# Optimization experiments

Hardware: AMD Instinct MI355X
Metric: run time of the kernel (lower is better)

## Reference

```python
import jax, jax.numpy as jnp
import numpy as np

D_MODEL = 1024
D_INNER = 2048
D_STATE = 16
D_CONV = 4
DT_RANK = 64  # ceil(d_model/16)


def _silu(v):
    return v * jax.nn.sigmoid(v)


def setup_inputs() -> dict:
    key = jax.random.key(0)
    ks = jax.random.split(key, 10)
    b, L = 2, 2048
    x = jax.random.normal(ks[0], (b, L, D_MODEL), jnp.float32)
    dt_vals = jax.random.uniform(ks[1], (b, L, 1), jnp.float32)
    W_in = jax.random.normal(ks[2], (D_MODEL, 2 * D_INNER), jnp.float32) * D_MODEL ** -0.5
    conv_w = jax.random.normal(ks[3], (D_INNER, D_CONV), jnp.float32) * D_CONV ** -0.5
    conv_b = jnp.zeros((D_INNER,), jnp.float32)
    W_x = jax.random.normal(ks[4], (D_INNER, DT_RANK + 2 * D_STATE), jnp.float32) * D_INNER ** -0.5
    std = DT_RANK ** -0.5
    W_dt = jax.random.uniform(ks[5], (1, D_INNER), jnp.float32, -std, std)
    dt = jnp.exp(jax.random.uniform(ks[6], (D_INNER,), jnp.float32)
                 * (np.log(0.1) - np.log(0.001)) + np.log(0.001))
    dt = jnp.clip(dt, 1e-4)
    b_dt = dt + jnp.log(-jnp.expm1(-dt))  # inverse-softplus init
    A_log = jnp.log(jnp.broadcast_to(jnp.arange(1, D_STATE + 1, dtype=jnp.float32),
                                     (D_INNER, D_STATE)))
    D_param = jnp.ones((D_INNER,), jnp.float32)
    W_out = jax.random.normal(ks[7], (D_INNER, D_MODEL), jnp.float32) * D_INNER ** -0.5
    return {"x": x, "dt_vals": dt_vals, "W_in": W_in, "conv_w": conv_w,
            "conv_b": conv_b, "W_x": W_x, "W_dt": W_dt, "b_dt": b_dt,
            "A_log": A_log, "D_param": D_param, "W_out": W_out}


def reference(x, dt_vals, W_in, conv_w, conv_b, W_x, W_dt, b_dt, A_log, D_param, W_out):
    b, L, _ = x.shape
    xz = x @ W_in                              # (b, L, 2*d_inner)
    xi, z = jnp.split(xz, 2, axis=-1)          # each (b, L, d_inner)
    # Causal depthwise conv1d (torch pads d_conv-1 both sides then slices [:seq])
    xp = jnp.pad(xi, ((0, 0), (D_CONV - 1, 0), (0, 0))).transpose(0, 2, 1)  # (b, di, L+k-1)
    xc = jax.lax.conv_general_dilated(
        xp, conv_w[:, None, :], window_strides=(1,), padding='VALID',
        dimension_numbers=('NCH', 'OIH', 'NCH'), feature_group_count=D_INNER)  # (b, di, L)
    xc = _silu(xc.transpose(0, 2, 1) + conv_b)  # (b, L, d_inner)

    x_dbl = xc @ W_x                            # (b, L, dt_rank + 2*d_state)
    Bm = x_dbl[..., DT_RANK:DT_RANK + D_STATE]  # (b, L, n)
    Cm = x_dbl[..., DT_RANK + D_STATE:]         # (b, L, n)
    delta = jax.nn.softplus(dt_vals @ W_dt + b_dt)  # (b, L, d_inner)
    A = -jnp.exp(A_log)                         # (d_inner, n)

    def step(h, t):
        d_t, x_t, B_t, C_t = t                  # (b,di) (b,di) (b,n) (b,n)
        h = jnp.exp(d_t[..., None] * A) * h + (d_t * x_t)[..., None] * B_t[:, None, :]
        y_t = jnp.einsum('bdn,bn->bd', h, C_t)
        return h, y_t

    h0 = jnp.zeros((b, D_INNER, D_STATE), xc.dtype)
    _, ys = jax.lax.scan(step, h0, (delta.transpose(1, 0, 2), xc.transpose(1, 0, 2),
                                    Bm.transpose(1, 0, 2), Cm.transpose(1, 0, 2)))
    y = ys.transpose(1, 0, 2) + D_param * xc    # skip term
    y = y * _silu(z)                            # gating
    return y @ W_out                            # (b, L, d_model)
```

## Files before the change

### kernel.cpp

```cpp
#include <hip/hip_runtime.h>
#include <math.h>

#define D_MODEL 1024
#define D_INNER 2048
#define D_STATE 16
#define D_CONVK 4
#define DT_RANK 64
#define BATCH   2
#define SEQ     2048
#define BL      (BATCH*SEQ)
#define NCHUNK  64
#define LOG2NC  6
#define CLEN    (SEQ/NCHUNK)
#define LOG2E   1.4426950408889634f

typedef __bf16 bf16x8 __attribute__((ext_vector_type(8)));
typedef float  f32x4  __attribute__((ext_vector_type(4)));

__device__ __forceinline__ float fexp2(float x){ return __builtin_exp2f(x); }
__device__ __forceinline__ float sigmoidf_(float x){
    return __builtin_amdgcn_rcpf(1.0f + __expf(-x));
}
__device__ __forceinline__ float softplusf_(float x){
    return (x > 20.0f) ? x : __logf(1.0f + __expf(x));
}
__device__ __forceinline__ unsigned short f2bf(float f){
    unsigned u = __float_as_uint(f);
    u += 0x7FFF + ((u >> 16) & 1);
    return (unsigned short)(u >> 16);
}
__device__ __forceinline__ float bf2f(unsigned short h){
    return __uint_as_float(((unsigned)h) << 16);
}
__device__ __forceinline__ void gload_lds16(const unsigned short* g, unsigned short* l){
    __builtin_amdgcn_global_load_lds(
        (const __attribute__((address_space(1))) unsigned int*)g,
        (__attribute__((address_space(3))) unsigned int*)l, 16, 0, 0);
}

__global__ __launch_bounds__(256)
void cvt_f32_bf16(const float* __restrict__ s, unsigned short* __restrict__ d, int n4){
    int i = blockIdx.x*256 + threadIdx.x;
    if (i >= n4) return;
    float4 v = ((const float4*)s)[i];
    ushort4 o;
    o.x = f2bf(v.x); o.y = f2bf(v.y); o.z = f2bf(v.z); o.w = f2bf(v.w);
    ((ushort4*)d)[i] = o;
}

__global__ __launch_bounds__(256)
void transpose_cvt(const float* __restrict__ src, unsigned short* __restrict__ dst,
                   int R, int C){
    __shared__ float t[32][33];
    int c0 = blockIdx.x*32, r0 = blockIdx.y*32;
    int tx = threadIdx.x & 31, ty = threadIdx.x >> 5;
#pragma unroll
    for (int i=0;i<32;i+=8) t[ty+i][tx] = src[(size_t)(r0+ty+i)*C + c0+tx];
    __syncthreads();
#pragma unroll
    for (int i=0;i<32;i+=8) dst[(size_t)(c0+ty+i)*R + r0+tx] = f2bf(t[tx][ty+i]);
}

__global__ __launch_bounds__(256)
void wx_prep(const float* __restrict__ Wx, unsigned short* __restrict__ wxT){
    int idx = blockIdx.x*256 + threadIdx.x;
    int k = idx & 2047, n = idx >> 11;
    wxT[(size_t)n*2048 + k] = f2bf(Wx[(size_t)k*96 + DT_RANK + n]);
}

template<int OUT_BF16>
__global__ __launch_bounds__(256)
void mfma_gemm_bt(const unsigned short* __restrict__ A,
                  const unsigned short* __restrict__ Bt,
                  void* __restrict__ C1v, void* __restrict__ C2v,
                  int lda, int ldc, int split, int kLen, size_t zStride)
{
    __shared__ __align__(16) unsigned short LDS[2*2*4096];
    const int tid = threadIdx.x;
    const int m0 = blockIdx.y * 128;
    const int n0 = blockIdx.x * 128;
    const int l  = tid & 63, w = tid >> 6;
    const int wr = (w >> 1) * 64, wc = (w & 1) * 64;
    const int fr = l & 15, kg = l >> 4;
    const int srow = tid >> 2;
    const int kcp  = tid & 3;
    const int kBegin = blockIdx.z * kLen;
    const int NT = kLen / 32;

    f32x4 acc[4][4];
    const f32x4 z4 = {0.f,0.f,0.f,0.f};
#pragma unroll
    for (int a=0;a<4;a++)
#pragma unroll
        for (int b=0;b<4;b++) acc[a][b] = z4;

    auto STAGE = [&](int buf, int k0){
#pragma unroll
        for (int i = 0; i < 2; ++i) {
            int rowA = i*64 + srow;
            int kcl  = kcp ^ ((rowA >> 1) & 3);
            gload_lds16(A  + (size_t)(m0 + rowA)*lda + k0 + kcl*8,
                        &LDS[buf*8192 +        i*2048 + w*512]);
            gload_lds16(Bt + (size_t)(n0 + rowA)*lda + k0 + kcl*8,
                        &LDS[buf*8192 + 4096 + i*2048 + w*512]);
        }
    };

    STAGE(0, kBegin);
    for (int t = 0; t < NT; ++t) {
        const int cur = t & 1;
        if (t + 1 < NT) {
            STAGE(cur ^ 1, kBegin + (t+1)*32);
            asm volatile("s_waitcnt vmcnt(4)" ::: "memory");
        } else {
            asm volatile("s_waitcnt vmcnt(0)" ::: "memory");
        }
        __builtin_amdgcn_s_barrier();

        bf16x8 af[4], bfv[4];
#pragma unroll
        for (int mr = 0; mr < 4; ++mr) {
            int r = wr + mr*16 + fr;
            af[mr] = *(const bf16x8*)&LDS[cur*8192 + r*32 + ((kg ^ ((r>>1)&3)))*8];
        }
#pragma unroll
        for (int nc = 0; nc < 4; ++nc) {
            int r = wc + nc*16 + fr;
            bfv[nc] = *(const bf16x8*)&LDS[cur*8192 + 4096 + r*32 + ((kg ^ ((r>>1)&3)))*8];
        }
#pragma unroll
        for (int mr = 0; mr < 4; ++mr)
#pragma unroll
            for (int nc = 0; nc < 4; ++nc)
                acc[mr][nc] = __builtin_amdgcn_mfma_f32_16x16x32_bf16(af[mr], bfv[nc], acc[mr][nc], 0, 0, 0);

        __builtin_amdgcn_s_barrier();
    }

    const int rg = l >> 4;
#pragma unroll
    for (int mr = 0; mr < 4; ++mr) {
#pragma unroll
        for (int nc = 0; nc < 4; ++nc) {
            int col = n0 + wc + nc*16 + fr;
            void* Cv; int cc;
            if (col < split) { Cv = C1v; cc = col; } else { Cv = C2v; cc = col - split; }
            int rbase = m0 + wr + mr*16 + rg*4;
            if (OUT_BF16) {
                unsigned short* Cb = (unsigned short*)Cv;
#pragma unroll
                for (int j = 0; j < 4; ++j)
                    Cb[(size_t)(rbase + j)*ldc + cc] = f2bf(acc[mr][nc][j]);
            } else {
                float* Cb = (float*)Cv + (size_t)blockIdx.z * zStride;
#pragma unroll
                for (int j = 0; j < 4; ++j)
                    Cb[(size_t)(rbase + j)*ldc + cc] = acc[mr][nc][j];
            }
        }
    }
}

__global__ __launch_bounds__(256)
void gemm2_bn64(const unsigned short* __restrict__ A,
                const unsigned short* __restrict__ Bt,
                float* __restrict__ P,
                int kLen, size_t zStride)
{
    __shared__ __align__(16) unsigned short LDS[3*6144];
    const int tid = threadIdx.x;
    const int m0 = blockIdx.y * 128;
    const int n0 = blockIdx.x * 64;
    const int l  = tid & 63, w = tid >> 6;
    const int wr = (w >> 1) * 64, wc = (w & 1) * 32;
    const int fr = l & 15, kg = l >> 4;
    const int srow = tid >> 2;
    const int kcp  = tid & 3;
    const int kBegin = blockIdx.z * kLen;
    const int NT = kLen / 32;

    f32x4 acc[4][2];
    const f32x4 z4 = {0.f,0.f,0.f,0.f};
#pragma unroll
    for (int a=0;a<4;a++){ acc[a][0]=z4; acc[a][1]=z4; }

    auto STAGE = [&](int buf, int k0){
#pragma unroll
        for (int i = 0; i < 2; ++i) {
            int rowA = i*64 + srow;
            int kcl  = kcp ^ ((rowA >> 1) & 3);
            gload_lds16(A + (size_t)(m0 + rowA)*2048 + k0 + kcl*8,
                        &LDS[buf*6144 + i*2048 + w*512]);
        }
        int kclB = kcp ^ ((srow >> 1) & 3);
        gload_lds16(Bt + (size_t)(n0 + srow)*2048 + k0 + kclB*8,
                    &LDS[buf*6144 + 4096 + w*512]);
    };

    STAGE(0, kBegin);
    STAGE(1, kBegin + 32);
    for (int t = 0; t < NT; ++t) {
        const int cur = t % 3;
        if (t + 2 < NT) {
            STAGE((t+2) % 3, kBegin + (t+2)*32);
            asm volatile("s_waitcnt vmcnt(6)" ::: "memory");
        } else if (t + 1 < NT) {
            asm volatile("s_waitcnt vmcnt(3)" ::: "memory");
        } else {
            asm volatile("s_waitcnt vmcnt(0)" ::: "memory");
        }
        __builtin_amdgcn_s_barrier();

        bf16x8 af[4], bfv[2];
#pragma unroll
        for (int mr = 0; mr < 4; ++mr) {
            int r = wr + mr*16 + fr;
            af[mr] = *(const bf16x8*)&LDS[cur*6144 + r*32 + ((kg ^ ((r>>1)&3)))*8];
        }
#pragma unroll
        for (int nc = 0; nc < 2; ++nc) {
            int r = wc + nc*16 + fr;
            bfv[nc] = *(const bf16x8*)&LDS[cur*6144 + 4096 + r*32 + ((kg ^ ((r>>1)&3)))*8];
        }
#pragma unroll
        for (int mr = 0; mr < 4; ++mr)
#pragma unroll
            for (int nc = 0; nc < 2; ++nc)
                acc[mr][nc] = __builtin_amdgcn_mfma_f32_16x16x32_bf16(af[mr], bfv[nc], acc[mr][nc], 0, 0, 0);

        __builtin_amdgcn_s_barrier();
    }

    const int rg = l >> 4;
    float* Cb = P + (size_t)blockIdx.z * zStride;
#pragma unroll
    for (int mr = 0; mr < 4; ++mr) {
#pragma unroll
        for (int nc = 0; nc < 2; ++nc) {
            int col   = n0 + wc + nc*16 + fr;
            int rbase = m0 + wr + mr*16 + rg*4;
#pragma unroll
            for (int j = 0; j < 4; ++j)
                Cb[(size_t)(rbase + j)*D_MODEL + col] = acc[mr][nc][j];
        }
    }
}

__global__ __launch_bounds__(256)
void bc_mfma(const unsigned short* __restrict__ A,
             const unsigned short* __restrict__ Bt,
             float* __restrict__ P)
{
    __shared__ __align__(16) unsigned short As[128*32];
    __shared__ __align__(16) unsigned short Bs[32*32];
    const int tid = threadIdx.x;
    const int m0 = blockIdx.x * 128;
    const int z  = blockIdx.y;
    const int l = tid & 63, w = tid >> 6;
    const int fr = l & 15, kg = l >> 4;

    f32x4 acc[2][2];
    const f32x4 z4 = {0.f,0.f,0.f,0.f};
    acc[0][0]=z4; acc[0][1]=z4; acc[1][0]=z4; acc[1][1]=z4;

    const int srow = tid >> 2;
    const int kcp  = tid & 3;
    const int kBegin = z * (D_INNER/8);

    for (int k0 = kBegin; k0 < kBegin + D_INNER/8; k0 += 32) {
        __syncthreads();
#pragma unroll
        for (int i = 0; i < 2; ++i) {
            int rowA = i*64 + srow;
            int kcl  = kcp ^ ((rowA >> 1) & 3);
            gload_lds16(A + (size_t)(m0 + rowA)*D_INNER + k0 + kcl*8, &As[i*2048 + w*512]);
        }
        if (w < 2) {
            int rowB = tid >> 2;
            int kcl  = kcp ^ ((rowB >> 1) & 3);
            gload_lds16(Bt + (size_t)rowB*D_INNER + k0 + kcl*8, &Bs[w*512]);
        }
        __syncthreads();

        bf16x8 af[2], bfv[2];
#pragma unroll
        for (int mr = 0; mr < 2; ++mr) {
            int r = w*32 + mr*16 + fr;
            af[mr] = *(const bf16x8*)&As[r*32 + ((kg ^ ((r>>1)&3)))*8];
        }
#pragma unroll
        for (int nc = 0; nc < 2; ++nc) {
            int r = nc*16 + fr;
            bfv[nc] = *(const bf16x8*)&Bs[r*32 + ((kg ^ ((r>>1)&3)))*8];
        }
#pragma unroll
        for (int mr = 0; mr < 2; ++mr)
#pragma unroll
            for (int nc = 0; nc < 2; ++nc)
                acc[mr][nc] = __builtin_amdgcn_mfma_f32_16x16x32_bf16(af[mr], bfv[nc], acc[mr][nc], 0, 0, 0);
    }

    const int rg = l >> 4;
    float* Pz = P + (size_t)z * BL * 32;
#pragma unroll
    for (int mr = 0; mr < 2; ++mr)
#pragma unroll
        for (int nc = 0; nc < 2; ++nc) {
            int rbase = m0 + w*32 + mr*16 + rg*4;
            int col   = nc*16 + fr;
#pragma unroll
            for (int j = 0; j < 4; ++j)
                Pz[(size_t)(rbase + j)*32 + col] = acc[mr][nc][j];
        }
}

__global__ __launch_bounds__(256)
void bc_reduce(const float* __restrict__ P, float* __restrict__ BC){
    int i = blockIdx.x*256 + threadIdx.x;
    if (i >= BL*32/4) return;
    float4 s = ((const float4*)P)[i];
#pragma unroll
    for (int zz = 1; zz < 8; ++zz) {
        float4 v = ((const float4*)P)[(size_t)zz*(BL*32/4) + i];
        s.x += v.x; s.y += v.y; s.z += v.z; s.w += v.w;
    }
    ((float4*)BC)[i] = s;
}

__global__ __launch_bounds__(256)
void add2_kernel(const float* __restrict__ P, float* __restrict__ out, size_t zStride, int n4){
    int i = blockIdx.x*256 + threadIdx.x;
    if (i >= n4) return;
    float4 a = ((const float4*)P)[i];
    float4 b = ((const float4*)(P + zStride))[i];
    float4 o; o.x=a.x+b.x; o.y=a.y+b.y; o.z=a.z+b.z; o.w=a.w+b.w;
    ((float4*)out)[i] = o;
}

__global__ __launch_bounds__(256)
void conv_silu_kernel(const unsigned short* __restrict__ xi_b, const float* __restrict__ conv_w,
                      const float* __restrict__ conv_b, unsigned short* __restrict__ xcb)
{
    int idx = blockIdx.x*256 + threadIdx.x;
    int dg  = idx & (D_INNER/4 - 1);
    int bt  = idx >> 9;
    int d   = dg*4;
    int t   = bt & (SEQ-1);
    float4 cw[4];
#pragma unroll
    for (int j=0;j<4;j++) cw[j] = *(const float4*)&conv_w[(d+j)*4];
    float s0 = conv_b[d], s1 = conv_b[d+1], s2 = conv_b[d+2], s3 = conv_b[d+3];
#pragma unroll
    for (int k=0;k<D_CONVK;k++){
        int tt = t - 3 + k;
        if (tt >= 0){
            ushort4 v = *(const ushort4*)&xi_b[(size_t)(bt-3+k)*D_INNER + d];
            s0 = fmaf(bf2f(v.x), ((const float*)&cw[0])[k], s0);
            s1 = fmaf(bf2f(v.y), ((const float*)&cw[1])[k], s1);
            s2 = fmaf(bf2f(v.z), ((const float*)&cw[2])[k], s2);
            s3 = fmaf(bf2f(v.w), ((const float*)&cw[3])[k], s3);
        }
    }
    ushort4 o;
    o.x = f2bf(s0 * sigmoidf_(s0));
    o.y = f2bf(s1 * sigmoidf_(s1));
    o.z = f2bf(s2 * sigmoidf_(s2));
    o.w = f2bf(s3 * sigmoidf_(s3));
    *(ushort4*)&xcb[(size_t)bt*D_INNER + d] = o;
}

__global__ __launch_bounds__(256)
void scan_passA(const unsigned short* __restrict__ xcb, const float* __restrict__ BC,
                const float* __restrict__ dt_vals, const float* __restrict__ W_dt,
                const float* __restrict__ b_dt, float* __restrict__ cs)
{
    const int db = blockIdx.x & 7;
    const int c  = (blockIdx.x >> 3) & (NCHUNK-1);
    const int b  = blockIdx.x >> (3 + LOG2NC);
    const int d  = db*256 + threadIdx.x;

    float wdt = W_dt[d], bdt = b_dt[d];

    float h[16];
#pragma unroll
    for (int n=0;n<16;n++) h[n]=0.0f;
    float S = 0.0f;

    const int tbase = b*SEQ + c*CLEN;
#pragma unroll
    for (int tt=0; tt<CLEN; ++tt){
        int bt = tbase + tt;
        float dv    = dt_vals[bt];
        float delta = softplusf_(fmaf(dv, wdt, bdt));
        S += delta;
        float xt = bf2f(xcb[(size_t)bt*D_INNER + d]);
        float dx = delta*xt;
        const float* Bp = &BC[(size_t)bt*32];
        float q = fexp2(-delta*LOG2E);
        float a = q;
#pragma unroll
        for (int n=0;n<16;n++){
            h[n] = fmaf(a, h[n], dx*Bp[n]);
            a *= q;
        }
    }
    size_t base = ((size_t)(b*NCHUNK + c))*17*D_INNER + d;
#pragma unroll
    for (int n=0;n<16;n++) cs[base + (size_t)n*D_INNER] = h[n];
    cs[base + (size_t)16*D_INNER] = S;
}

__global__ __launch_bounds__(256)
void combine_kernel(const float* __restrict__ A_log, float* __restrict__ cs)
{
    int gid = blockIdx.x*256 + threadIdx.x;
    int d = gid & (D_INNER-1);
    int n = (gid >> 11) & 15;
    int b = gid >> 15;
    float Ad2 = -__expf(A_log[d*16+n]) * LOG2E;
    const size_t stride = (size_t)17*D_INNER;
    size_t base = (size_t)(b*NCHUNK)*stride + d;
    float hs = 0.0f;
    size_t hoff = (size_t)n*D_INNER, soff = (size_t)16*D_INNER;
    float h_cur = cs[base + hoff];
    float S_cur = cs[base + soff];
#pragma unroll 8
    for (int c=0;c<NCHUNK-1;c++){
        float h_nxt = cs[base + stride + hoff];
        float S_nxt = cs[base + stride + soff];
        float ap = fexp2(Ad2*S_cur);
        cs[base + hoff] = hs;
        hs = fmaf(ap, hs, h_cur);
        h_cur = h_nxt; S_cur = S_nxt; base += stride;
    }
    cs[base + hoff] = hs;
}

__global__ __launch_bounds__(256)
void scan_passC(const unsigned short* __restrict__ xcb, const float* __restrict__ BC,
                const float* __restrict__ dt_vals, const float* __restrict__ W_dt,
                const float* __restrict__ b_dt, const float* __restrict__ D_param,
                const unsigned short* __restrict__ z_b,
                const float* __restrict__ cs, unsigned short* __restrict__ Ybf)
{
    const int db = blockIdx.x & 7;
    const int c  = (blockIdx.x >> 3) & (NCHUNK-1);
    const int b  = blockIdx.x >> (3 + LOG2NC);
    const int d  = db*256 + threadIdx.x;

    float wdt = W_dt[d], bdt = b_dt[d];
    float Dp  = D_param[d];

    float h[16];
    size_t base = ((size_t)(b*NCHUNK + c))*17*D_INNER + d;
#pragma unroll
    for (int n=0;n<16;n++) h[n] = cs[base + (size_t)n*D_INNER];

    const int tbase = b*SEQ + c*CLEN;
#pragma unroll
    for (int tt=0; tt<CLEN; ++tt){
        int bt = tbase + tt;
        float dv    = dt_vals[bt];
        float delta = softplusf_(fmaf(dv, wdt, bdt));
        float xt = bf2f(xcb[(size_t)bt*D_INNER + d]);
        float dx = delta*xt;
        const float* Bp = &BC[(size_t)bt*32];
        const float* Cp = Bp + 16;
        float q = fexp2(-delta*LOG2E);
        float a = q;
        float y = 0.0f;
#pragma unroll
        for (int n=0;n<16;n++){
            h[n] = fmaf(a, h[n], dx*Bp[n]);
            y    = fmaf(h[n], Cp[n], y);
            a *= q;
        }
        float zt  = bf2f(z_b[(size_t)bt*D_INNER + d]);
        float outv = fmaf(Dp, xt, y) * zt * sigmoidf_(zt);
        Ybf[(size_t)bt*D_INNER + d] = f2bf(outv);
    }
}

extern "C" void kernel_launch(void* const* d_in, const int* in_sizes, int n_in,
                              void* d_out, int out_size, void* d_ws, size_t ws_size,
                              hipStream_t stream)
{
    const float* x       = (const float*)d_in[0];
    const float* dt_vals = (const float*)d_in[1];
    const float* W_in    = (const float*)d_in[2];
    const float* conv_w  = (const float*)d_in[3];
    const float* conv_b  = (const float*)d_in[4];
    const float* W_x     = (const float*)d_in[5];
    const float* W_dt    = (const float*)d_in[6];
    const float* b_dt    = (const float*)d_in[7];
    const float* A_log   = (const float*)d_in[8];
    const float* D_param = (const float*)d_in[9];
    const float* W_out   = (const float*)d_in[10];
    float* out = (float*)d_out;

    char* W = (char*)d_ws;
    size_t o = 0;
    unsigned short* xi_b = (unsigned short*)(W + o); o += (size_t)BL*D_INNER*2;
    unsigned short* z_b  = (unsigned short*)(W + o); o += (size_t)BL*D_INNER*2;
    unsigned short* xcb  = (unsigned short*)(W + o); o += (size_t)BL*D_INNER*2;
    unsigned short* ybf  = (unsigned short*)(W + o); o += (size_t)BL*D_INNER*2;
    float* BC    = (float*)(W + o);   o += (size_t)BL*32*4;
    unsigned short* woutT = (unsigned short*)(W + o); o += (size_t)D_MODEL*D_INNER*2;
    char* OV = W + o;
    unsigned short* xbf  = (unsigned short*)OV;
    unsigned short* winT = (unsigned short*)(OV + (size_t)BL*D_MODEL*2);
    float*          bcP  = (float*)OV;
    unsigned short* wxT  = (unsigned short*)(OV + (size_t)8*BL*32*4);
    float* cs = (float*)OV;
    float* Ppart = (float*)OV;

    const size_t zStrideG2 = (size_t)BL * D_MODEL;

    cvt_f32_bf16<<<(BL*D_MODEL/4+255)/256, 256, 0, stream>>>(x, xbf, BL*D_MODEL/4);
    transpose_cvt<<<dim3(2*D_INNER/32, D_MODEL/32), 256, 0, stream>>>(W_in, winT, D_MODEL, 2*D_INNER);
    mfma_gemm_bt<1><<<dim3(32,32), 256, 0, stream>>>(xbf, winT, xi_b, z_b,
                                                     D_MODEL, D_INNER, D_INNER, D_MODEL, 0);
    transpose_cvt<<<dim3(D_MODEL/32, D_INNER/32), 256, 0, stream>>>(W_out, woutT, D_INNER, D_MODEL);
    wx_prep<<<(32*D_INNER)/256, 256, 0, stream>>>(W_x, wxT);
    conv_silu_kernel<<<(BL*D_INNER/4)/256, 256, 0, stream>>>(xi_b, conv_w, conv_b, xcb);
    bc_mfma<<<dim3(BL/128, 8), 256, 0, stream>>>(xcb, wxT, bcP);
    bc_reduce<<<(BL*32/4+255)/256, 256, 0, stream>>>(bcP, BC);
    scan_passA<<<BATCH*NCHUNK*8, 256, 0, stream>>>(xcb, BC, dt_vals, W_dt, b_dt, cs);
    combine_kernel<<<(BATCH*16*D_INNER)/256, 256, 0, stream>>>(A_log, cs);
    scan_passC<<<BATCH*NCHUNK*8, 256, 0, stream>>>(xcb, BC, dt_vals, W_dt, b_dt,
                                                   D_param, z_b, cs, ybf);
    gemm2_bn64<<<dim3(D_MODEL/64, BL/128, 2), 256, 0, stream>>>(ybf, woutT, Ppart,
                                                                D_INNER/2, zStrideG2);
    add2_kernel<<<(BL*D_MODEL/4+255)/256, 256, 0, stream>>>(Ppart, out, zStrideG2, BL*D_MODEL/4);
}
```

Baseline: 202.1 us.

## Replace input projection GEMM with 256x256-tile, 4-stage pipelined MFMA kernel

The in-projection GEMM now uses 256x256 output tiles with 512 threads (8 waves, each computing 128x64), in place of 128x128 tiles with 256 threads. Global-to-LDS loads go through a 4-buffer ring with three stages in flight and graded vmcnt waits, which drops the trailing barrier of each iteration. MFMA issue is bracketed with s_setprio. The larger tile raises data reuse per LDS load and the deeper prefetch hides memory latency, at the cost of 128KB LDS, more registers, and only 256 blocks, which may leave the 256-CU device poorly balanced.

```diff
diff --git a/kernel.cpp b/kernel.cpp
--- a/kernel.cpp
+++ b/kernel.cpp
@@ -68,95 +68,84 @@
     wxT[(size_t)n*2048 + k] = f2bf(Wx[(size_t)k*96 + DT_RANK + n]);
 }
 
-template<int OUT_BF16>
-__global__ __launch_bounds__(256)
-void mfma_gemm_bt(const unsigned short* __restrict__ A,
-                  const unsigned short* __restrict__ Bt,
-                  void* __restrict__ C1v, void* __restrict__ C2v,
-                  int lda, int ldc, int split, int kLen, size_t zStride)
-{
-    __shared__ __align__(16) unsigned short LDS[2*2*4096];
+__global__ __launch_bounds__(512)
+void gemm1_256(const unsigned short* __restrict__ A,
+               const unsigned short* __restrict__ Bt,
+               unsigned short* __restrict__ C1,
+               unsigned short* __restrict__ C2,
+               int K)
+{
+    __shared__ __align__(16) unsigned short LDS[4*16384];
     const int tid = threadIdx.x;
-    const int m0 = blockIdx.y * 128;
-    const int n0 = blockIdx.x * 128;
-    const int l  = tid & 63, w = tid >> 6;
-    const int wr = (w >> 1) * 64, wc = (w & 1) * 64;
-    const int fr = l & 15, kg = l >> 4;
-    const int srow = tid >> 2;
-    const int kcp  = tid & 3;
-    const int kBegin = blockIdx.z * kLen;
-    const int NT = kLen / 32;
-
-    f32x4 acc[4][4];
+    const int l  = tid & 63, wv = tid >> 6;
+    const int wm = wv >> 2, wn = wv & 3;
+    const int fr = l & 15, kg = l >> 4, rg = kg;
+    const int m0 = blockIdx.y * 256;
+    const int n0 = blockIdx.x * 256;
+    const int NT = K / 32;
+
+    f32x4 acc[8][4];
     const f32x4 z4 = {0.f,0.f,0.f,0.f};
 #pragma unroll
-    for (int a=0;a<4;a++)
+    for (int a=0;a<8;a++)
 #pragma unroll
         for (int b=0;b<4;b++) acc[a][b] = z4;
 
     auto STAGE = [&](int buf, int k0){
 #pragma unroll
         for (int i = 0; i < 2; ++i) {
-            int rowA = i*64 + srow;
-            int kcl  = kcp ^ ((rowA >> 1) & 3);
-            gload_lds16(A  + (size_t)(m0 + rowA)*lda + k0 + kcl*8,
-                        &LDS[buf*8192 +        i*2048 + w*512]);
-            gload_lds16(Bt + (size_t)(n0 + rowA)*lda + k0 + kcl*8,
-                        &LDS[buf*8192 + 4096 + i*2048 + w*512]);
+            int off = (i*8 + wv)*64 + l;
+            int row = off >> 2;
+            int kcl = (off & 3) ^ ((row >> 1) & 3);
+            gload_lds16(A  + (size_t)(m0+row)*K + k0 + kcl*8,
+                        &LDS[buf*16384 + (i*8+wv)*512]);
+            gload_lds16(Bt + (size_t)(n0+row)*K + k0 + kcl*8,
+                        &LDS[buf*16384 + 8192 + (i*8+wv)*512]);
         }
     };
 
-    STAGE(0, kBegin);
+    STAGE(0, 0); STAGE(1, 32); STAGE(2, 64);
     for (int t = 0; t < NT; ++t) {
-        const int cur = t & 1;
-        if (t + 1 < NT) {
-            STAGE(cur ^ 1, kBegin + (t+1)*32);
-            asm volatile("s_waitcnt vmcnt(4)" ::: "memory");
-        } else {
-            asm volatile("s_waitcnt vmcnt(0)" ::: "memory");
-        }
+        if (t < NT-2)       asm volatile("s_waitcnt vmcnt(8)" ::: "memory");
+        else if (t == NT-2) asm volatile("s_waitcnt vmcnt(4)" ::: "memory");
+        else                asm volatile("s_waitcnt vmcnt(0)" ::: "memory");
         __builtin_amdgcn_s_barrier();
 
-        bf16x8 af[4], bfv[4];
-#pragma unroll
-        for (int mr = 0; mr < 4; ++mr) {
-            int r = wr + mr*16 + fr;
-            af[mr] = *(const bf16x8*)&LDS[cur*8192 + r*32 + ((kg ^ ((r>>1)&3)))*8];
+        const unsigned short* Ab = &LDS[(t & 3)*16384];
+        const unsigned short* Bb = Ab + 8192;
+        bf16x8 af[8], bfr[4];
+#pragma unroll
+        for (int mr = 0; mr < 8; ++mr) {
+            int r = wm*128 + mr*16 + fr;
+            af[mr] = *(const bf16x8*)&Ab[r*32 + ((kg ^ ((r>>1)&3)))*8];
         }
 #pragma unroll
         for (int nc = 0; nc < 4; ++nc) {
-            int r = wc + nc*16 + fr;
-            bfv[nc] = *(const bf16x8*)&LDS[cur*8192 + 4096 + r*32 + ((kg ^ ((r>>1)&3)))*8];
-        }
-#pragma unroll
-        for (int mr = 0; mr < 4; ++mr)
+            int r = wn*64 + nc*16 + fr;
+            bfr[nc] = *(const bf16x8*)&Bb[r*32 + ((kg ^ ((r>>1)&3)))*8];
+        }
+        if (t + 3 < NT) STAGE((t+3) & 3, (t+3)*32);
+
+        __builtin_amdgcn_s_setprio(1);
+#pragma unroll
+        for (int mr = 0; mr < 8; ++mr)
 #pragma unroll
             for (int nc = 0; nc < 4; ++nc)
-                acc[mr][nc] = __builtin_amdgcn_mfma_f32_16x16x32_bf16(af[mr], bfv[nc], acc[mr][nc], 0, 0, 0);
-
-        __builtin_amdgcn_s_barrier();
-    }
-
-    const int rg = l >> 4;
-#pragma unroll
-    for (int mr = 0; mr < 4; ++mr) {
+                acc[mr][nc] = __builtin_amdgcn_mfma_f32_16x16x32_bf16(af[mr], bfr[nc], acc[mr][nc], 0, 0, 0);
+        __builtin_amdgcn_s_setprio(0);
+    }
+
+    unsigned short* Cb; int coff;
+    if (n0 < D_INNER) { Cb = C1; coff = n0; } else { Cb = C2; coff = n0 - D_INNER; }
+#pragma unroll
+    for (int mr = 0; mr < 8; ++mr) {
 #pragma unroll
         for (int nc = 0; nc < 4; ++nc) {
-            int col = n0 + wc + nc*16 + fr;
-            void* Cv; int cc;
-            if (col < split) { Cv = C1v; cc = col; } else { Cv = C2v; cc = col - split; }
-            int rbase = m0 + wr + mr*16 + rg*4;
-            if (OUT_BF16) {
-                unsigned short* Cb = (unsigned short*)Cv;
-#pragma unroll
-                for (int j = 0; j < 4; ++j)
-                    Cb[(size_t)(rbase + j)*ldc + cc] = f2bf(acc[mr][nc][j]);
-            } else {
-                float* Cb = (float*)Cv + (size_t)blockIdx.z * zStride;
-#pragma unroll
-                for (int j = 0; j < 4; ++j)
-                    Cb[(size_t)(rbase + j)*ldc + cc] = acc[mr][nc][j];
-            }
+            int cc = coff + wn*64 + nc*16 + fr;
+            int rb = m0 + wm*128 + mr*16 + rg*4;
+#pragma unroll
+            for (int j = 0; j < 4; ++j)
+                Cb[(size_t)(rb + j)*D_INNER + cc] = f2bf(acc[mr][nc][j]);
         }
     }
 }
@@ -518,8 +507,7 @@
 
     cvt_f32_bf16<<<(BL*D_MODEL/4+255)/256, 256, 0, stream>>>(x, xbf, BL*D_MODEL/4);
     transpose_cvt<<<dim3(2*D_INNER/32, D_MODEL/32), 256, 0, stream>>>(W_in, winT, D_MODEL, 2*D_INNER);
-    mfma_gemm_bt<1><<<dim3(32,32), 256, 0, stream>>>(xbf, winT, xi_b, z_b,
-                                                     D_MODEL, D_INNER, D_INNER, D_MODEL, 0);
+    gemm1_256<<<dim3((2*D_INNER)/256, BL/256), 512, 0, stream>>>(xbf, winT, xi_b, z_b, D_MODEL);
     transpose_cvt<<<dim3(D_MODEL/32, D_INNER/32), 256, 0, stream>>>(W_out, woutT, D_INNER, D_MODEL);
     wx_prep<<<(32*D_INNER)/256, 256, 0, stream>>>(W_x, wxT);
     conv_silu_kernel<<<(BL*D_INNER/4)/256, 256, 0, stream>>>(xi_b, conv_w, conv_b, xcb);
```

Measured after the change: 197.2 us. 2.4% less time.
